# Kernel optimization log

Measured on AMD Instinct MI355X. Metric: run time of the kernel, lower is better.

Reference implementation:

```python
import jax, jax.numpy as jnp
import numpy as np

NUM_HEADS = 32
HEAD_DIM = 128
NUM_KV_HEADS = 8
SCALING = HEAD_DIM ** -0.5


def setup_inputs() -> dict:
    key = jax.random.key(0)
    kq, kk, kv = jax.random.split(key, 3)
    B, S = 2, 2048
    return {
        "query": jax.random.normal(kq, (B, S, NUM_HEADS * HEAD_DIM), dtype=jnp.float32),
        "key": jax.random.normal(kk, (B, S, NUM_KV_HEADS * HEAD_DIM), dtype=jnp.float32),
        "value": jax.random.normal(kv, (B, S, NUM_KV_HEADS * HEAD_DIM), dtype=jnp.float32),
    }


def reference(query, key, value):
    B, S, _ = query.shape
    n_rep = NUM_HEADS // NUM_KV_HEADS
    # [B, H, S, D]
    q = query.reshape(B, S, NUM_HEADS, HEAD_DIM).transpose(0, 2, 1, 3)
    k = key.reshape(B, S, NUM_KV_HEADS, HEAD_DIM).transpose(0, 2, 1, 3)
    v = value.reshape(B, S, NUM_KV_HEADS, HEAD_DIM).transpose(0, 2, 1, 3)
    # repeat_kv: (B, Hkv, S, D) -> (B, Hkv*n_rep, S, D)
    k = jnp.repeat(k, n_rep, axis=1)
    v = jnp.repeat(v, n_rep, axis=1)
    # attention scores [B, H, S, S]
    scores = jnp.einsum("bhqd,bhkd->bhqk", q, k) * SCALING
    causal = jnp.tril(jnp.ones((S, S), dtype=bool))
    scores = jnp.where(causal, scores, -jnp.inf)
    # softmax in fp32, cast back to query dtype
    attn = jax.nn.softmax(scores.astype(jnp.float32), axis=-1).astype(q.dtype)
    out = jnp.einsum("bhqk,bhkd->bhqd", attn, v)
    # back to [B, S, H*D]
    return out.transpose(0, 2, 1, 3).reshape(B, S, NUM_HEADS * HEAD_DIM)
```

## Files before the change

kernel.cpp:

```cpp
#include <hip/hip_runtime.h>

#define B_    2
#define S_    2048
#define H_    32
#define KVH_  8
#define D_    128
#define QB    128
#define KB    64
#define NT_   (S_ / KB)
#define SCALE2 0.12751743f
#define THR2  8.0f

typedef short  short8 __attribute__((ext_vector_type(8)));
typedef float  f32x4  __attribute__((ext_vector_type(4)));

__device__ inline unsigned short f2bf(float f) {
    unsigned int u = __float_as_uint(f);
    u += 0x7fffu + ((u >> 16) & 1u);
    return (unsigned short)(u >> 16);
}
__device__ __forceinline__ float exp2_fast(float x) {
    float r; asm("v_exp_f32 %0, %1" : "=v"(r) : "v"(x)); return r;
}
__device__ __forceinline__ unsigned int cvt_pk_bf16(float lo, float hi) {
    unsigned int r;
    asm("v_cvt_pk_bf16_f32 %0, %1, %2" : "=v"(r) : "v"(lo), "v"(hi));
    return r;
}

__global__ void prep_kernel(const float* __restrict__ k, const float* __restrict__ v,
                            unsigned short* __restrict__ kfb,
                            unsigned short* __restrict__ vfb) {
    __shared__ unsigned short Kt[64][136];
    __shared__ unsigned short Vt[64][132];
    const int t = threadIdx.x;
    const int kt = blockIdx.x, bkvh = blockIdx.y;
    const int b = bkvh >> 3, kvh = bkvh & 7;
    const size_t rs = KVH_ * D_;
    const float* ks = k + ((size_t)(b * S_ + kt * 64)) * rs + kvh * D_;
    const float* vs = v + ((size_t)(b * S_ + kt * 64)) * rs + kvh * D_;
    #pragma unroll
    for (int i = 0; i < 8; ++i) {
        const int row = (t >> 5) + i * 8;
        const int col = (t & 31) * 4;
        const float4 a = *(const float4*)(ks + (size_t)row * rs + col);
        const float4 c = *(const float4*)(vs + (size_t)row * rs + col);
        ushort4 wa, wc;
        wa.x = f2bf(a.x); wa.y = f2bf(a.y); wa.z = f2bf(a.z); wa.w = f2bf(a.w);
        wc.x = f2bf(c.x); wc.y = f2bf(c.y); wc.z = f2bf(c.z); wc.w = f2bf(c.w);
        *(ushort4*)&Kt[row][col] = wa;
        *(ushort4*)&Vt[row][col] = wc;
    }
    __syncthreads();
    const int lane = t & 63, m16 = lane & 15, quad = lane >> 4;
    unsigned short* kout = kfb + (size_t)(bkvh * NT_ + kt) * 16 * 512;
    unsigned short* vout = vfb + (size_t)(bkvh * NT_ + kt) * 16 * 512;
    #pragma unroll
    for (int i = 0; i < 4; ++i) {
        const int g = (t >> 6) * 4 + i;
        const int c = g >> 2, nt = g & 3;
        const short8 kk = *(const short8*)&Kt[nt * 16 + m16][c * 32 + quad * 8];
        *(short8*)(kout + g * 512 + lane * 8) = kk;
        const int c2 = g >> 3, dn = g & 7;
        short8 vv;
        #pragma unroll
        for (int j = 0; j < 8; ++j)
            vv[j] = (short)Vt[c2 * 32 + quad * 8 + j][dn * 16 + m16];
        *(short8*)(vout + g * 512 + lane * 8) = vv;
    }
}

#define KV_TILE_B 16384
#define BUF_B     32768
#define PSH_OFF   65536
#define SMEM_B    (PSH_OFF + 128 * 64 * 2)

__device__ __forceinline__ void gld16(const void* g, void* l) {
    __builtin_amdgcn_global_load_lds(
        (const __attribute__((address_space(1))) unsigned int*)g,
        (__attribute__((address_space(3))) unsigned int*)l, 16, 0, 0);
}

__global__ __launch_bounds__(512, 4) void fa9_kernel(
    const float* __restrict__ q, const unsigned short* __restrict__ kfb,
    const unsigned short* __restrict__ vfb, float* __restrict__ out) {

    __shared__ __align__(16) char smem[SMEM_B];
    unsigned short* Psh = (unsigned short*)(smem + PSH_OFF);

    const int t    = threadIdx.x;
    const int wave = t >> 6;
    const int lane = t & 63;
    const int m16  = lane & 15;
    const int quad = lane >> 4;

    const int bh  = blockIdx.y;
    const int b   = bh >> 5;
    const int h   = bh & 31;
    const int kvh = h >> 2;

    const char* kB = (const char*)kfb + (size_t)(b * KVH_ + kvh) * NT_ * KV_TILE_B;
    const char* vB = (const char*)vfb + (size_t)(b * KVH_ + kvh) * NT_ * KV_TILE_B;

    const int prow_base = (wave * 16 + m16) * 64;
    unsigned short* pw[4];
    #pragma unroll
    for (int nt = 0; nt < 4; ++nt)
        pw[nt] = Psh + prow_base + (((nt * 2 + (quad >> 1)) ^ (m16 & 7)) << 3) + (quad & 1) * 4;
    const unsigned short* pr0 = Psh + prow_base + (((quad)     ^ (m16 & 7)) << 3);
    const unsigned short* pr1 = Psh + prow_base + (((4 + quad) ^ (m16 & 7)) << 3);

    for (int half = 0; half < 2; ++half) {
        const int qtile = half ? (int)blockIdx.x : (S_ / QB - 1 - (int)blockIdx.x);
        const int qbase = qtile * QB;
        const int ktmax = 2 * qtile + 1;
        const int qrow  = qbase + wave * 16 + m16;

        if (half) __syncthreads();

        #pragma unroll
        for (int r = 0; r < 2; ++r) {
            gld16(kB + r * 8192 + t * 16, smem + r * 8192 + t * 16);
            gld16(vB + r * 8192 + t * 16, smem + KV_TILE_B + r * 8192 + t * 16);
        }

        short8 qf[4];
        {
            const float* qp = q + (size_t)(b * S_ + qrow) * (H_ * D_) + h * D_;
            #pragma unroll
            for (int c = 0; c < 4; ++c) {
                const float4 x0 = *(const float4*)(qp + c * 32 + quad * 8);
                const float4 x1 = *(const float4*)(qp + c * 32 + quad * 8 + 4);
                short8 f;
                f[0] = (short)f2bf(x0.x * SCALE2); f[1] = (short)f2bf(x0.y * SCALE2);
                f[2] = (short)f2bf(x0.z * SCALE2); f[3] = (short)f2bf(x0.w * SCALE2);
                f[4] = (short)f2bf(x1.x * SCALE2); f[5] = (short)f2bf(x1.y * SCALE2);
                f[6] = (short)f2bf(x1.z * SCALE2); f[7] = (short)f2bf(x1.w * SCALE2);
                qf[c] = f;
            }
        }

        f32x4 o[8];
        #pragma unroll
        for (int i = 0; i < 8; ++i) o[i] = (f32x4){0.f, 0.f, 0.f, 0.f};
        float m_q = -INFINITY, l_q = 0.f;

        __syncthreads();

        for (int ktt = 0; ktt <= ktmax; ++ktt) {
            const int kb  = ktt * KB;
            const int cur = ktt & 1;

            if (ktt < ktmax) {
                char* dst = smem + (cur ^ 1) * BUF_B + t * 16;
                const char* ks = kB + (size_t)(ktt + 1) * KV_TILE_B + t * 16;
                const char* vs = vB + (size_t)(ktt + 1) * KV_TILE_B + t * 16;
                #pragma unroll
                for (int r = 0; r < 2; ++r) {
                    gld16(ks + r * 8192, dst + r * 8192);
                    gld16(vs + r * 8192, dst + KV_TILE_B + r * 8192);
                }
            }
            const unsigned short* Kl = (const unsigned short*)(smem + cur * BUF_B);
            const unsigned short* Vl = Kl + KV_TILE_B / 2;

            f32x4 sa[4];
            #pragma unroll
            for (int nt = 0; nt < 4; ++nt) sa[nt] = (f32x4){0.f, 0.f, 0.f, 0.f};
            #pragma unroll
            for (int c = 0; c < 4; ++c) {
                short8 kf[4];
                #pragma unroll
                for (int nt = 0; nt < 4; ++nt)
                    kf[nt] = *(const short8*)(Kl + (c * 4 + nt) * 512 + lane * 8);
                #pragma unroll
                for (int nt = 0; nt < 4; ++nt)
                    sa[nt] = __builtin_amdgcn_mfma_f32_16x16x32_bf16(kf[nt], qf[c], sa[nt], 0, 0, 0);
            }

            const bool dodiag = (ktt >= 2 * qtile);
            float p[4][4];
            #pragma unroll
            for (int nt = 0; nt < 4; ++nt) {
                #pragma unroll
                for (int r = 0; r < 4; ++r) {
                    float sv = sa[nt][r];
                    if (dodiag) {
                        const int keyg = kb + nt * 16 + quad * 4 + r;
                        if (keyg > qrow) sv = -INFINITY;
                    }
                    p[nt][r] = sv;
                }
            }
            float mv;
            {
                float t0 = fmaxf(fmaxf(p[0][0], p[0][1]), fmaxf(p[0][2], p[0][3]));
                float t1 = fmaxf(fmaxf(p[1][0], p[1][1]), fmaxf(p[1][2], p[1][3]));
                float t2 = fmaxf(fmaxf(p[2][0], p[2][1]), fmaxf(p[2][2], p[2][3]));
                float t3 = fmaxf(fmaxf(p[3][0], p[3][1]), fmaxf(p[3][2], p[3][3]));
                mv = fmaxf(fmaxf(t0, t1), fmaxf(t2, t3));
                mv = fmaxf(mv, __shfl_xor(mv, 16));
                mv = fmaxf(mv, __shfl_xor(mv, 32));
            }
            if (__any(mv - m_q > THR2)) {
                const float mnew = fmaxf(m_q, mv);
                const float al = exp2_fast(m_q - mnew);
                m_q = mnew;
                l_q *= al;
                float alo[4];
                #pragma unroll
                for (int r = 0; r < 4; ++r)
                    alo[r] = __shfl(al, quad * 20 + r);
                #pragma unroll
                for (int dn = 0; dn < 8; ++dn)
                    #pragma unroll
                    for (int r = 0; r < 4; ++r) o[dn][r] *= alo[r];
            }
            #pragma unroll
            for (int nt = 0; nt < 4; ++nt) {
                const float e0 = exp2_fast(p[nt][0] - m_q);
                const float e1 = exp2_fast(p[nt][1] - m_q);
                const float e2 = exp2_fast(p[nt][2] - m_q);
                const float e3 = exp2_fast(p[nt][3] - m_q);
                l_q += (e0 + e1) + (e2 + e3);
                uint2 w;
                w.x = cvt_pk_bf16(e0, e1);
                w.y = cvt_pk_bf16(e2, e3);
                *(uint2*)pw[nt] = w;
            }
            asm volatile("s_waitcnt lgkmcnt(0)" ::: "memory");
            short8 pf[2];
            pf[0] = *(const short8*)pr0;
            pf[1] = *(const short8*)pr1;

            #pragma unroll
            for (int dn = 0; dn < 8; ++dn) {
                const short8 vv = *(const short8*)(Vl + dn * 512 + lane * 8);
                o[dn] = __builtin_amdgcn_mfma_f32_16x16x32_bf16(pf[0], vv, o[dn], 0, 0, 0);
            }
            #pragma unroll
            for (int dn = 0; dn < 8; ++dn) {
                const short8 vv = *(const short8*)(Vl + (8 + dn) * 512 + lane * 8);
                o[dn] = __builtin_amdgcn_mfma_f32_16x16x32_bf16(pf[1], vv, o[dn], 0, 0, 0);
            }

            __syncthreads();
        }

        float ls = l_q;
        ls += __shfl_xor(ls, 16);
        ls += __shfl_xor(ls, 32);
        const float inv_q = 1.f / ls;
        float inv[4];
        #pragma unroll
        for (int r = 0; r < 4; ++r)
            inv[r] = __shfl(inv_q, quad * 20 + r);

        float* Ot = (float*)smem + wave * (16 * 128);
        #pragma unroll
        for (int dn = 0; dn < 8; ++dn)
            #pragma unroll
            for (int r = 0; r < 4; ++r)
                Ot[(quad * 4 + r) * 128 + dn * 16 + m16] = o[dn][r] * inv[r];
        asm volatile("s_waitcnt lgkmcnt(0)" ::: "memory");
        float* og = out + (size_t)(b * S_ + qbase + wave * 16) * (H_ * D_) + h * D_;
        #pragma unroll
        for (int i = 0; i < 8; ++i) {
            const int row = (lane >> 5) + i * 2;
            const int col = (lane & 31) * 4;
            *(float4*)(og + (size_t)row * (H_ * D_) + col) = *(const float4*)(Ot + row * 128 + col);
        }
    }
}

extern "C" void kernel_launch(void* const* d_in, const int* in_sizes, int n_in,
                              void* d_out, int out_size, void* d_ws, size_t ws_size,
                              hipStream_t stream) {
    const float* q = (const float*)d_in[0];
    const float* k = (const float*)d_in[1];
    const float* v = (const float*)d_in[2];
    float* out = (float*)d_out;

    unsigned short* kfb = (unsigned short*)d_ws;
    unsigned short* vfb = (unsigned short*)d_ws + (size_t)B_ * KVH_ * S_ * D_;

    prep_kernel<<<dim3(NT_, B_ * KVH_), dim3(256), 0, stream>>>(k, v, kfb, vfb);
    fa9_kernel<<<dim3(S_ / QB / 2, B_ * H_), dim3(512), 0, stream>>>(q, kfb, vfb, out);
}
```

Baseline: 225.9 us.

## Restructure attention to 4-wave blocks with two query row-blocks per wave and 32-key tiles

The attention kernel drops from 8 waves to 4 waves per block. Each wave now handles two 16-row query blocks that share each K/V fragment load, and keys are streamed in 32-key sub-tiles with a smaller double buffer. The prep kernel is split so each block handles 32 keys, and the output layout is reordered to match. The paired-qtile load balancing is removed: each block processes one q tile, heaviest first. s_setprio is added around the MFMA sections. The aim is more fragment reuse per LDS read and less LDS per block. The costs are more register pressure, more loop iterations and barriers, and causal imbalance between blocks.

```diff
diff --git a/kernel.cpp b/kernel.cpp
--- a/kernel.cpp
+++ b/kernel.cpp
@@ -6,8 +6,7 @@
 #define KVH_  8
 #define D_    128
 #define QB    128
-#define KB    64
-#define NT_   (S_ / KB)
+#define NT_   (S_ / 64)
 #define SCALE2 0.12751743f
 #define THR2  8.0f
 
@@ -31,16 +30,17 @@
 __global__ void prep_kernel(const float* __restrict__ k, const float* __restrict__ v,
                             unsigned short* __restrict__ kfb,
                             unsigned short* __restrict__ vfb) {
-    __shared__ unsigned short Kt[64][136];
-    __shared__ unsigned short Vt[64][132];
+    __shared__ unsigned short Kt[32][136];
+    __shared__ unsigned short Vt[32][132];
     const int t = threadIdx.x;
-    const int kt = blockIdx.x, bkvh = blockIdx.y;
+    const int kt64 = blockIdx.x >> 1, sub = blockIdx.x & 1;
+    const int bkvh = blockIdx.y;
     const int b = bkvh >> 3, kvh = bkvh & 7;
     const size_t rs = KVH_ * D_;
-    const float* ks = k + ((size_t)(b * S_ + kt * 64)) * rs + kvh * D_;
-    const float* vs = v + ((size_t)(b * S_ + kt * 64)) * rs + kvh * D_;
-    #pragma unroll
-    for (int i = 0; i < 8; ++i) {
+    const float* ks = k + ((size_t)(b * S_ + kt64 * 64 + sub * 32)) * rs + kvh * D_;
+    const float* vs = v + ((size_t)(b * S_ + kt64 * 64 + sub * 32)) * rs + kvh * D_;
+    #pragma unroll
+    for (int i = 0; i < 4; ++i) {
         const int row = (t >> 5) + i * 8;
         const int col = (t & 31) * 4;
         const float4 a = *(const float4*)(ks + (size_t)row * rs + col);
@@ -53,27 +53,29 @@
     }
     __syncthreads();
     const int lane = t & 63, m16 = lane & 15, quad = lane >> 4;
-    unsigned short* kout = kfb + (size_t)(bkvh * NT_ + kt) * 16 * 512;
-    unsigned short* vout = vfb + (size_t)(bkvh * NT_ + kt) * 16 * 512;
-    #pragma unroll
-    for (int i = 0; i < 4; ++i) {
-        const int g = (t >> 6) * 4 + i;
-        const int c = g >> 2, nt = g & 3;
-        const short8 kk = *(const short8*)&Kt[nt * 16 + m16][c * 32 + quad * 8];
-        *(short8*)(kout + g * 512 + lane * 8) = kk;
-        const int c2 = g >> 3, dn = g & 7;
+    const int w = t >> 6;
+    unsigned short* kout = kfb + (size_t)(bkvh * NT_ + kt64) * 16 * 512;
+    unsigned short* vout = vfb + (size_t)(bkvh * NT_ + kt64) * 16 * 512;
+    #pragma unroll
+    for (int ntl = 0; ntl < 2; ++ntl) {
+        const short8 kk = *(const short8*)&Kt[ntl * 16 + m16][w * 32 + quad * 8];
+        *(short8*)(kout + (w * 4 + sub * 2 + ntl) * 512 + lane * 8) = kk;
+    }
+    #pragma unroll
+    for (int i = 0; i < 2; ++i) {
+        const int dn = w * 2 + i;
         short8 vv;
         #pragma unroll
         for (int j = 0; j < 8; ++j)
-            vv[j] = (short)Vt[c2 * 32 + quad * 8 + j][dn * 16 + m16];
-        *(short8*)(vout + g * 512 + lane * 8) = vv;
-    }
-}
-
-#define KV_TILE_B 16384
-#define BUF_B     32768
-#define PSH_OFF   65536
-#define SMEM_B    (PSH_OFF + 128 * 64 * 2)
+            vv[j] = (short)Vt[quad * 8 + j][dn * 16 + m16];
+        *(short8*)(vout + (sub * 8 + dn) * 512 + lane * 8) = vv;
+    }
+}
+
+#define TILE64_B 16384
+#define BUF_B    16384
+#define PSH_OFF  32768
+#define SMEM_B   (PSH_OFF + 128 * 64 * 2)
 
 __device__ __forceinline__ void gld16(const void* g, void* l) {
     __builtin_amdgcn_global_load_lds(
@@ -81,7 +83,7 @@
         (__attribute__((address_space(3))) unsigned int*)l, 16, 0, 0);
 }
 
-__global__ __launch_bounds__(512, 4) void fa9_kernel(
+__global__ __launch_bounds__(256, 3) void fa10_kernel(
     const float* __restrict__ q, const unsigned short* __restrict__ kfb,
     const unsigned short* __restrict__ vfb, float* __restrict__ out) {
 
@@ -94,119 +96,125 @@
     const int m16  = lane & 15;
     const int quad = lane >> 4;
 
+    const int qtile = 15 - (int)blockIdx.x;
+    const int qbase = qtile * QB;
+    const int ktmax = 4 * qtile + 3;
+
     const int bh  = blockIdx.y;
     const int b   = bh >> 5;
     const int h   = bh & 31;
     const int kvh = h >> 2;
 
-    const char* kB = (const char*)kfb + (size_t)(b * KVH_ + kvh) * NT_ * KV_TILE_B;
-    const char* vB = (const char*)vfb + (size_t)(b * KVH_ + kvh) * NT_ * KV_TILE_B;
-
-    const int prow_base = (wave * 16 + m16) * 64;
-    unsigned short* pw[4];
-    #pragma unroll
-    for (int nt = 0; nt < 4; ++nt)
-        pw[nt] = Psh + prow_base + (((nt * 2 + (quad >> 1)) ^ (m16 & 7)) << 3) + (quad & 1) * 4;
-    const unsigned short* pr0 = Psh + prow_base + (((quad)     ^ (m16 & 7)) << 3);
-    const unsigned short* pr1 = Psh + prow_base + (((4 + quad) ^ (m16 & 7)) << 3);
-
-    for (int half = 0; half < 2; ++half) {
-        const int qtile = half ? (int)blockIdx.x : (S_ / QB - 1 - (int)blockIdx.x);
-        const int qbase = qtile * QB;
-        const int ktmax = 2 * qtile + 1;
-        const int qrow  = qbase + wave * 16 + m16;
-
-        if (half) __syncthreads();
-
-        #pragma unroll
-        for (int r = 0; r < 2; ++r) {
-            gld16(kB + r * 8192 + t * 16, smem + r * 8192 + t * 16);
-            gld16(vB + r * 8192 + t * 16, smem + KV_TILE_B + r * 8192 + t * 16);
-        }
-
-        short8 qf[4];
-        {
-            const float* qp = q + (size_t)(b * S_ + qrow) * (H_ * D_) + h * D_;
+    const char* kB = (const char*)kfb + (size_t)(b * KVH_ + kvh) * NT_ * TILE64_B;
+    const char* vB = (const char*)vfb + (size_t)(b * KVH_ + kvh) * NT_ * TILE64_B;
+
+    const int inner = lane * 16;
+    const int g0 = wave;
+    const int kst0 = ((g0 >> 1) * 4 + (g0 & 1)) * 1024 + inner;
+    const int kst1 = (((g0 + 4) >> 1) * 4 + ((g0 + 4) & 1)) * 1024 + inner;
+
+    const int psh_row0 = (wave * 16 + m16) * 64;
+    unsigned short* pw0 = Psh + psh_row0 + ((((quad >> 1))     ^ (m16 & 7)) << 3) + (quad & 1) * 4;
+    unsigned short* pw1 = Psh + psh_row0 + (((2 + (quad >> 1)) ^ (m16 & 7)) << 3) + (quad & 1) * 4;
+    const unsigned short* pr = Psh + psh_row0 + ((quad ^ (m16 & 7)) << 3);
+
+    gld16(kB + kst0,          smem + t * 16);
+    gld16(kB + kst1,          smem + 4096 + t * 16);
+    gld16(vB + t * 16,        smem + 8192 + t * 16);
+    gld16(vB + 4096 + t * 16, smem + 12288 + t * 16);
+
+    const int qr0 = qbase + wave * 16 + m16;
+    const int qr1 = qr0 + 64;
+    short8 qf[2][4];
+    #pragma unroll
+    for (int rb = 0; rb < 2; ++rb) {
+        const float* qp = q + (size_t)(b * S_ + (rb ? qr1 : qr0)) * (H_ * D_) + h * D_;
+        #pragma unroll
+        for (int c = 0; c < 4; ++c) {
+            const float4 x0 = *(const float4*)(qp + c * 32 + quad * 8);
+            const float4 x1 = *(const float4*)(qp + c * 32 + quad * 8 + 4);
+            short8 f;
+            f[0] = (short)f2bf(x0.x * SCALE2); f[1] = (short)f2bf(x0.y * SCALE2);
+            f[2] = (short)f2bf(x0.z * SCALE2); f[3] = (short)f2bf(x0.w * SCALE2);
+            f[4] = (short)f2bf(x1.x * SCALE2); f[5] = (short)f2bf(x1.y * SCALE2);
+            f[6] = (short)f2bf(x1.z * SCALE2); f[7] = (short)f2bf(x1.w * SCALE2);
+            qf[rb][c] = f;
+        }
+    }
+
+    f32x4 o[2][8];
+    #pragma unroll
+    for (int rb = 0; rb < 2; ++rb)
+        #pragma unroll
+        for (int i = 0; i < 8; ++i) o[rb][i] = (f32x4){0.f, 0.f, 0.f, 0.f};
+    float m_q[2] = {-INFINITY, -INFINITY}, l_q[2] = {0.f, 0.f};
+
+    __syncthreads();
+
+    for (int ktt = 0; ktt <= ktmax; ++ktt) {
+        const int kb  = ktt * 32;
+        const int cur = ktt & 1;
+
+        if (ktt < ktmax) {
+            const int n = ktt + 1;
+            const char* kt_ = kB + (size_t)(n >> 1) * TILE64_B + (n & 1) * 2048;
+            const char* vt_ = vB + (size_t)(n >> 1) * TILE64_B + (n & 1) * 8192;
+            char* dst = smem + (n & 1) * BUF_B;
+            gld16(kt_ + kst0,          dst + t * 16);
+            gld16(kt_ + kst1,          dst + 4096 + t * 16);
+            gld16(vt_ + t * 16,        dst + 8192 + t * 16);
+            gld16(vt_ + 4096 + t * 16, dst + 12288 + t * 16);
+        }
+        const unsigned short* Kl = (const unsigned short*)(smem + cur * BUF_B);
+        const unsigned short* Vl = Kl + 4096;
+
+        f32x4 sa[2][2];
+        #pragma unroll
+        for (int rb = 0; rb < 2; ++rb)
             #pragma unroll
-            for (int c = 0; c < 4; ++c) {
-                const float4 x0 = *(const float4*)(qp + c * 32 + quad * 8);
-                const float4 x1 = *(const float4*)(qp + c * 32 + quad * 8 + 4);
-                short8 f;
-                f[0] = (short)f2bf(x0.x * SCALE2); f[1] = (short)f2bf(x0.y * SCALE2);
-                f[2] = (short)f2bf(x0.z * SCALE2); f[3] = (short)f2bf(x0.w * SCALE2);
-                f[4] = (short)f2bf(x1.x * SCALE2); f[5] = (short)f2bf(x1.y * SCALE2);
-                f[6] = (short)f2bf(x1.z * SCALE2); f[7] = (short)f2bf(x1.w * SCALE2);
-                qf[c] = f;
-            }
-        }
-
-        f32x4 o[8];
-        #pragma unroll
-        for (int i = 0; i < 8; ++i) o[i] = (f32x4){0.f, 0.f, 0.f, 0.f};
-        float m_q = -INFINITY, l_q = 0.f;
-
-        __syncthreads();
-
-        for (int ktt = 0; ktt <= ktmax; ++ktt) {
-            const int kb  = ktt * KB;
-            const int cur = ktt & 1;
-
-            if (ktt < ktmax) {
-                char* dst = smem + (cur ^ 1) * BUF_B + t * 16;
-                const char* ks = kB + (size_t)(ktt + 1) * KV_TILE_B + t * 16;
-                const char* vs = vB + (size_t)(ktt + 1) * KV_TILE_B + t * 16;
-                #pragma unroll
-                for (int r = 0; r < 2; ++r) {
-                    gld16(ks + r * 8192, dst + r * 8192);
-                    gld16(vs + r * 8192, dst + KV_TILE_B + r * 8192);
-                }
-            }
-            const unsigned short* Kl = (const unsigned short*)(smem + cur * BUF_B);
-            const unsigned short* Vl = Kl + KV_TILE_B / 2;
-
-            f32x4 sa[4];
+            for (int ntl = 0; ntl < 2; ++ntl) sa[rb][ntl] = (f32x4){0.f, 0.f, 0.f, 0.f};
+        __builtin_amdgcn_s_setprio(1);
+        #pragma unroll
+        for (int c = 0; c < 4; ++c) {
+            const short8 kf0 = *(const short8*)(Kl + (c * 2)     * 512 + lane * 8);
+            const short8 kf1 = *(const short8*)(Kl + (c * 2 + 1) * 512 + lane * 8);
+            sa[0][0] = __builtin_amdgcn_mfma_f32_16x16x32_bf16(kf0, qf[0][c], sa[0][0], 0, 0, 0);
+            sa[0][1] = __builtin_amdgcn_mfma_f32_16x16x32_bf16(kf1, qf[0][c], sa[0][1], 0, 0, 0);
+            sa[1][0] = __builtin_amdgcn_mfma_f32_16x16x32_bf16(kf0, qf[1][c], sa[1][0], 0, 0, 0);
+            sa[1][1] = __builtin_amdgcn_mfma_f32_16x16x32_bf16(kf1, qf[1][c], sa[1][1], 0, 0, 0);
+        }
+        __builtin_amdgcn_s_setprio(0);
+
+        #pragma unroll
+        for (int rb = 0; rb < 2; ++rb) {
+            const bool dodiag = (ktt >= 4 * qtile + 2 * rb);
+            const int  qr = rb ? qr1 : qr0;
+            float p[2][4];
             #pragma unroll
-            for (int nt = 0; nt < 4; ++nt) sa[nt] = (f32x4){0.f, 0.f, 0.f, 0.f};
-            #pragma unroll
-            for (int c = 0; c < 4; ++c) {
-                short8 kf[4];
-                #pragma unroll
-                for (int nt = 0; nt < 4; ++nt)
-                    kf[nt] = *(const short8*)(Kl + (c * 4 + nt) * 512 + lane * 8);
-                #pragma unroll
-                for (int nt = 0; nt < 4; ++nt)
-                    sa[nt] = __builtin_amdgcn_mfma_f32_16x16x32_bf16(kf[nt], qf[c], sa[nt], 0, 0, 0);
-            }
-
-            const bool dodiag = (ktt >= 2 * qtile);
-            float p[4][4];
-            #pragma unroll
-            for (int nt = 0; nt < 4; ++nt) {
+            for (int ntl = 0; ntl < 2; ++ntl) {
                 #pragma unroll
                 for (int r = 0; r < 4; ++r) {
-                    float sv = sa[nt][r];
+                    float sv = sa[rb][ntl][r];
                     if (dodiag) {
-                        const int keyg = kb + nt * 16 + quad * 4 + r;
-                        if (keyg > qrow) sv = -INFINITY;
+                        const int keyg = kb + ntl * 16 + quad * 4 + r;
+                        if (keyg > qr) sv = -INFINITY;
                     }
-                    p[nt][r] = sv;
+                    p[ntl][r] = sv;
                 }
             }
             float mv;
             {
-                float t0 = fmaxf(fmaxf(p[0][0], p[0][1]), fmaxf(p[0][2], p[0][3]));
-                float t1 = fmaxf(fmaxf(p[1][0], p[1][1]), fmaxf(p[1][2], p[1][3]));
-                float t2 = fmaxf(fmaxf(p[2][0], p[2][1]), fmaxf(p[2][2], p[2][3]));
-                float t3 = fmaxf(fmaxf(p[3][0], p[3][1]), fmaxf(p[3][2], p[3][3]));
-                mv = fmaxf(fmaxf(t0, t1), fmaxf(t2, t3));
+                const float t0 = fmaxf(fmaxf(p[0][0], p[0][1]), fmaxf(p[0][2], p[0][3]));
+                const float t1 = fmaxf(fmaxf(p[1][0], p[1][1]), fmaxf(p[1][2], p[1][3]));
+                mv = fmaxf(t0, t1);
                 mv = fmaxf(mv, __shfl_xor(mv, 16));
                 mv = fmaxf(mv, __shfl_xor(mv, 32));
             }
-            if (__any(mv - m_q > THR2)) {
-                const float mnew = fmaxf(m_q, mv);
-                const float al = exp2_fast(m_q - mnew);
-                m_q = mnew;
-                l_q *= al;
+            if (__any(mv - m_q[rb] > THR2)) {
+                const float mnew = fmaxf(m_q[rb], mv);
+                const float al = exp2_fast(m_q[rb] - mnew);
+                m_q[rb] = mnew;
+                l_q[rb] *= al;
                 float alo[4];
                 #pragma unroll
                 for (int r = 0; r < 4; ++r)
@@ -214,40 +222,47 @@
                 #pragma unroll
                 for (int dn = 0; dn < 8; ++dn)
                     #pragma unroll
-                    for (int r = 0; r < 4; ++r) o[dn][r] *= alo[r];
+                    for (int r = 0; r < 4; ++r) o[rb][dn][r] *= alo[r];
             }
-            #pragma unroll
-            for (int nt = 0; nt < 4; ++nt) {
-                const float e0 = exp2_fast(p[nt][0] - m_q);
-                const float e1 = exp2_fast(p[nt][1] - m_q);
-                const float e2 = exp2_fast(p[nt][2] - m_q);
-                const float e3 = exp2_fast(p[nt][3] - m_q);
-                l_q += (e0 + e1) + (e2 + e3);
-                uint2 w;
-                w.x = cvt_pk_bf16(e0, e1);
-                w.y = cvt_pk_bf16(e2, e3);
-                *(uint2*)pw[nt] = w;
+            {
+                const float e0 = exp2_fast(p[0][0] - m_q[rb]);
+                const float e1 = exp2_fast(p[0][1] - m_q[rb]);
+                const float e2 = exp2_fast(p[0][2] - m_q[rb]);
+                const float e3 = exp2_fast(p[0][3] - m_q[rb]);
+                const float f0 = exp2_fast(p[1][0] - m_q[rb]);
+                const float f1 = exp2_fast(p[1][1] - m_q[rb]);
+                const float f2 = exp2_fast(p[1][2] - m_q[rb]);
+                const float f3 = exp2_fast(p[1][3] - m_q[rb]);
+                l_q[rb] += ((e0 + e1) + (e2 + e3)) + ((f0 + f1) + (f2 + f3));
+                uint2 w0, w1;
+                w0.x = cvt_pk_bf16(e0, e1); w0.y = cvt_pk_bf16(e2, e3);
+                w1.x = cvt_pk_bf16(f0, f1); w1.y = cvt_pk_bf16(f2, f3);
+                *(uint2*)(pw0 + rb * 4096) = w0;
+                *(uint2*)(pw1 + rb * 4096) = w1;
             }
-            asm volatile("s_waitcnt lgkmcnt(0)" ::: "memory");
-            short8 pf[2];
-            pf[0] = *(const short8*)pr0;
-            pf[1] = *(const short8*)pr1;
-
-            #pragma unroll
-            for (int dn = 0; dn < 8; ++dn) {
-                const short8 vv = *(const short8*)(Vl + dn * 512 + lane * 8);
-                o[dn] = __builtin_amdgcn_mfma_f32_16x16x32_bf16(pf[0], vv, o[dn], 0, 0, 0);
-            }
-            #pragma unroll
-            for (int dn = 0; dn < 8; ++dn) {
-                const short8 vv = *(const short8*)(Vl + (8 + dn) * 512 + lane * 8);
-                o[dn] = __builtin_amdgcn_mfma_f32_16x16x32_bf16(pf[1], vv, o[dn], 0, 0, 0);
-            }
-
-            __syncthreads();
-        }
-
-        float ls = l_q;
+        }
+
+        asm volatile("s_waitcnt lgkmcnt(0)" ::: "memory");
+        short8 pf[2];
+        pf[0] = *(const short8*)pr;
+        pf[1] = *(const short8*)(pr + 4096);
+
+        __builtin_amdgcn_s_setprio(1);
+        #pragma unroll
+        for (int dn = 0; dn < 8; ++dn) {
+            const short8 vv = *(const short8*)(Vl + dn * 512 + lane * 8);
+            o[0][dn] = __builtin_amdgcn_mfma_f32_16x16x32_bf16(pf[0], vv, o[0][dn], 0, 0, 0);
+            o[1][dn] = __builtin_amdgcn_mfma_f32_16x16x32_bf16(pf[1], vv, o[1][dn], 0, 0, 0);
+        }
+        __builtin_amdgcn_s_setprio(0);
+
+        __syncthreads();
+    }
+
+    float* Ot = (float*)smem + wave * 2048;
+    #pragma unroll
+    for (int rb = 0; rb < 2; ++rb) {
+        float ls = l_q[rb];
         ls += __shfl_xor(ls, 16);
         ls += __shfl_xor(ls, 32);
         const float inv_q = 1.f / ls;
@@ -255,15 +270,13 @@
         #pragma unroll
         for (int r = 0; r < 4; ++r)
             inv[r] = __shfl(inv_q, quad * 20 + r);
-
-        float* Ot = (float*)smem + wave * (16 * 128);
         #pragma unroll
         for (int dn = 0; dn < 8; ++dn)
             #pragma unroll
             for (int r = 0; r < 4; ++r)
-                Ot[(quad * 4 + r) * 128 + dn * 16 + m16] = o[dn][r] * inv[r];
+                Ot[(quad * 4 + r) * 128 + dn * 16 + m16] = o[rb][dn][r] * inv[r];
         asm volatile("s_waitcnt lgkmcnt(0)" ::: "memory");
-        float* og = out + (size_t)(b * S_ + qbase + wave * 16) * (H_ * D_) + h * D_;
+        float* og = out + (size_t)(b * S_ + qbase + rb * 64 + wave * 16) * (H_ * D_) + h * D_;
         #pragma unroll
         for (int i = 0; i < 8; ++i) {
             const int row = (lane >> 5) + i * 2;
@@ -284,6 +297,6 @@
     unsigned short* kfb = (unsigned short*)d_ws;
     unsigned short* vfb = (unsigned short*)d_ws + (size_t)B_ * KVH_ * S_ * D_;
 
-    prep_kernel<<<dim3(NT_, B_ * KVH_), dim3(256), 0, stream>>>(k, v, kfb, vfb);
-    fa9_kernel<<<dim3(S_ / QB / 2, B_ * H_), dim3(512), 0, stream>>>(q, kfb, vfb, out);
-}
+    prep_kernel<<<dim3(NT_ * 2, B_ * KVH_), dim3(256), 0, stream>>>(k, v, kfb, vfb);
+    fa10_kernel<<<dim3(16, B_ * H_), dim3(256), 0, stream>>>(q, kfb, vfb, out);
+}
```

Result: slower. 302.6 us (+33.9%).

## Halve waves per block, each wave computes two 16-row query sub-blocks

Applied to the files above, without the earlier changes.

The block drops from 8 waves to 4 and each wave now handles two 16-row query blocks (rows r and r+64). Every K and V fragment read from LDS therefore feeds two MFMAs, halving LDS traffic per FLOP, and the causal mask is applied per sub-block. MFMA sections are wrapped in s_setprio to favour matrix issue. The cost is roughly double the accumulator and score registers per wave and fewer waves to hide latency. Launch bounds change to (256,2) to match.

```diff
diff --git a/kernel.cpp b/kernel.cpp
--- a/kernel.cpp
+++ b/kernel.cpp
@@ -6,8 +6,7 @@
 #define KVH_  8
 #define D_    128
 #define QB    128
-#define KB    64
-#define NT_   (S_ / KB)
+#define NT_   (S_ / 64)
 #define SCALE2 0.12751743f
 #define THR2  8.0f
 
@@ -70,10 +69,10 @@
     }
 }
 
-#define KV_TILE_B 16384
-#define BUF_B     32768
-#define PSH_OFF   65536
-#define SMEM_B    (PSH_OFF + 128 * 64 * 2)
+#define TILE_B  16384
+#define BUF_B   32768
+#define PSH_OFF 65536
+#define SMEM_B  (PSH_OFF + 128 * 64 * 2)
 
 __device__ __forceinline__ void gld16(const void* g, void* l) {
     __builtin_amdgcn_global_load_lds(
@@ -81,7 +80,7 @@
         (__attribute__((address_space(3))) unsigned int*)l, 16, 0, 0);
 }
 
-__global__ __launch_bounds__(512, 4) void fa9_kernel(
+__global__ __launch_bounds__(256, 2) void fa11_kernel(
     const float* __restrict__ q, const unsigned short* __restrict__ kfb,
     const unsigned short* __restrict__ vfb, float* __restrict__ out) {
 
@@ -99,34 +98,36 @@
     const int h   = bh & 31;
     const int kvh = h >> 2;
 
-    const char* kB = (const char*)kfb + (size_t)(b * KVH_ + kvh) * NT_ * KV_TILE_B;
-    const char* vB = (const char*)vfb + (size_t)(b * KVH_ + kvh) * NT_ * KV_TILE_B;
-
-    const int prow_base = (wave * 16 + m16) * 64;
+    const char* kB = (const char*)kfb + (size_t)(b * KVH_ + kvh) * NT_ * TILE_B;
+    const char* vB = (const char*)vfb + (size_t)(b * KVH_ + kvh) * NT_ * TILE_B;
+
+    const int psh_row = (wave * 16 + m16) * 64;
     unsigned short* pw[4];
     #pragma unroll
     for (int nt = 0; nt < 4; ++nt)
-        pw[nt] = Psh + prow_base + (((nt * 2 + (quad >> 1)) ^ (m16 & 7)) << 3) + (quad & 1) * 4;
-    const unsigned short* pr0 = Psh + prow_base + (((quad)     ^ (m16 & 7)) << 3);
-    const unsigned short* pr1 = Psh + prow_base + (((4 + quad) ^ (m16 & 7)) << 3);
+        pw[nt] = Psh + psh_row + (((nt * 2 + (quad >> 1)) ^ (m16 & 7)) << 3) + (quad & 1) * 4;
+    const unsigned short* pr0 = Psh + psh_row + (((quad)     ^ (m16 & 7)) << 3);
+    const unsigned short* pr1 = Psh + psh_row + (((4 + quad) ^ (m16 & 7)) << 3);
 
     for (int half = 0; half < 2; ++half) {
-        const int qtile = half ? (int)blockIdx.x : (S_ / QB - 1 - (int)blockIdx.x);
+        const int qtile = half ? (int)blockIdx.x : (15 - (int)blockIdx.x);
         const int qbase = qtile * QB;
         const int ktmax = 2 * qtile + 1;
-        const int qrow  = qbase + wave * 16 + m16;
 
         if (half) __syncthreads();
 
         #pragma unroll
-        for (int r = 0; r < 2; ++r) {
-            gld16(kB + r * 8192 + t * 16, smem + r * 8192 + t * 16);
-            gld16(vB + r * 8192 + t * 16, smem + KV_TILE_B + r * 8192 + t * 16);
+        for (int r = 0; r < 4; ++r) {
+            gld16(kB + r * 4096 + t * 16, smem + r * 4096 + t * 16);
+            gld16(vB + r * 4096 + t * 16, smem + 16384 + r * 4096 + t * 16);
         }
 
-        short8 qf[4];
-        {
-            const float* qp = q + (size_t)(b * S_ + qrow) * (H_ * D_) + h * D_;
+        const int qr0 = qbase + wave * 16 + m16;
+        const int qr1 = qr0 + 64;
+        short8 qf[2][4];
+        #pragma unroll
+        for (int rb = 0; rb < 2; ++rb) {
+            const float* qp = q + (size_t)(b * S_ + (rb ? qr1 : qr0)) * (H_ * D_) + h * D_;
             #pragma unroll
             for (int c = 0; c < 4; ++c) {
                 const float4 x0 = *(const float4*)(qp + c * 32 + quad * 8);
@@ -136,37 +137,42 @@
                 f[2] = (short)f2bf(x0.z * SCALE2); f[3] = (short)f2bf(x0.w * SCALE2);
                 f[4] = (short)f2bf(x1.x * SCALE2); f[5] = (short)f2bf(x1.y * SCALE2);
                 f[6] = (short)f2bf(x1.z * SCALE2); f[7] = (short)f2bf(x1.w * SCALE2);
-                qf[c] = f;
+                qf[rb][c] = f;
             }
         }
 
-        f32x4 o[8];
-        #pragma unroll
-        for (int i = 0; i < 8; ++i) o[i] = (f32x4){0.f, 0.f, 0.f, 0.f};
-        float m_q = -INFINITY, l_q = 0.f;
+        f32x4 o[2][8];
+        #pragma unroll
+        for (int rb = 0; rb < 2; ++rb)
+            #pragma unroll
+            for (int i = 0; i < 8; ++i) o[rb][i] = (f32x4){0.f, 0.f, 0.f, 0.f};
+        float m_q[2] = {-INFINITY, -INFINITY}, l_q[2] = {0.f, 0.f};
 
         __syncthreads();
 
         for (int ktt = 0; ktt <= ktmax; ++ktt) {
-            const int kb  = ktt * KB;
+            const int kb  = ktt * 64;
             const int cur = ktt & 1;
 
             if (ktt < ktmax) {
+                const char* ks = kB + (size_t)(ktt + 1) * TILE_B + t * 16;
+                const char* vs = vB + (size_t)(ktt + 1) * TILE_B + t * 16;
                 char* dst = smem + (cur ^ 1) * BUF_B + t * 16;
-                const char* ks = kB + (size_t)(ktt + 1) * KV_TILE_B + t * 16;
-                const char* vs = vB + (size_t)(ktt + 1) * KV_TILE_B + t * 16;
-                #pragma unroll
-                for (int r = 0; r < 2; ++r) {
-                    gld16(ks + r * 8192, dst + r * 8192);
-                    gld16(vs + r * 8192, dst + KV_TILE_B + r * 8192);
+                #pragma unroll
+                for (int r = 0; r < 4; ++r) {
+                    gld16(ks + r * 4096, dst + r * 4096);
+                    gld16(vs + r * 4096, dst + 16384 + r * 4096);
                 }
             }
             const unsigned short* Kl = (const unsigned short*)(smem + cur * BUF_B);
-            const unsigned short* Vl = Kl + KV_TILE_B / 2;
-
-            f32x4 sa[4];
-            #pragma unroll
-            for (int nt = 0; nt < 4; ++nt) sa[nt] = (f32x4){0.f, 0.f, 0.f, 0.f};
+            const unsigned short* Vl = Kl + 8192;
+
+            f32x4 sa[2][4];
+            #pragma unroll
+            for (int rb = 0; rb < 2; ++rb)
+                #pragma unroll
+                for (int nt = 0; nt < 4; ++nt) sa[rb][nt] = (f32x4){0.f, 0.f, 0.f, 0.f};
+            __builtin_amdgcn_s_setprio(1);
             #pragma unroll
             for (int c = 0; c < 4; ++c) {
                 short8 kf[4];
@@ -174,101 +180,114 @@
                 for (int nt = 0; nt < 4; ++nt)
                     kf[nt] = *(const short8*)(Kl + (c * 4 + nt) * 512 + lane * 8);
                 #pragma unroll
-                for (int nt = 0; nt < 4; ++nt)
-                    sa[nt] = __builtin_amdgcn_mfma_f32_16x16x32_bf16(kf[nt], qf[c], sa[nt], 0, 0, 0);
-            }
-
-            const bool dodiag = (ktt >= 2 * qtile);
-            float p[4][4];
-            #pragma unroll
-            for (int nt = 0; nt < 4; ++nt) {
-                #pragma unroll
-                for (int r = 0; r < 4; ++r) {
-                    float sv = sa[nt][r];
-                    if (dodiag) {
-                        const int keyg = kb + nt * 16 + quad * 4 + r;
-                        if (keyg > qrow) sv = -INFINITY;
+                for (int nt = 0; nt < 4; ++nt) {
+                    sa[0][nt] = __builtin_amdgcn_mfma_f32_16x16x32_bf16(kf[nt], qf[0][c], sa[0][nt], 0, 0, 0);
+                    sa[1][nt] = __builtin_amdgcn_mfma_f32_16x16x32_bf16(kf[nt], qf[1][c], sa[1][nt], 0, 0, 0);
+                }
+            }
+            __builtin_amdgcn_s_setprio(0);
+
+            #pragma unroll
+            for (int rb = 0; rb < 2; ++rb) {
+                const bool dodiag = (ktt >= 2 * qtile + rb);
+                const int  qr = rb ? qr1 : qr0;
+                float p[4][4];
+                #pragma unroll
+                for (int nt = 0; nt < 4; ++nt) {
+                    #pragma unroll
+                    for (int r = 0; r < 4; ++r) {
+                        float sv = sa[rb][nt][r];
+                        if (dodiag) {
+                            const int keyg = kb + nt * 16 + quad * 4 + r;
+                            if (keyg > qr) sv = -INFINITY;
+                        }
+                        p[nt][r] = sv;
                     }
-                    p[nt][r] = sv;
-                }
-            }
-            float mv;
-            {
-                float t0 = fmaxf(fmaxf(p[0][0], p[0][1]), fmaxf(p[0][2], p[0][3]));
-                float t1 = fmaxf(fmaxf(p[1][0], p[1][1]), fmaxf(p[1][2], p[1][3]));
-                float t2 = fmaxf(fmaxf(p[2][0], p[2][1]), fmaxf(p[2][2], p[2][3]));
-                float t3 = fmaxf(fmaxf(p[3][0], p[3][1]), fmaxf(p[3][2], p[3][3]));
-                mv = fmaxf(fmaxf(t0, t1), fmaxf(t2, t3));
-                mv = fmaxf(mv, __shfl_xor(mv, 16));
-                mv = fmaxf(mv, __shfl_xor(mv, 32));
-            }
-            if (__any(mv - m_q > THR2)) {
-                const float mnew = fmaxf(m_q, mv);
-                const float al = exp2_fast(m_q - mnew);
-                m_q = mnew;
-                l_q *= al;
-                float alo[4];
-                #pragma unroll
-                for (int r = 0; r < 4; ++r)
-                    alo[r] = __shfl(al, quad * 20 + r);
-                #pragma unroll
-                for (int dn = 0; dn < 8; ++dn)
+                }
+                float mv;
+                {
+                    const float t0 = fmaxf(fmaxf(p[0][0], p[0][1]), fmaxf(p[0][2], p[0][3]));
+                    const float t1 = fmaxf(fmaxf(p[1][0], p[1][1]), fmaxf(p[1][2], p[1][3]));
+                    const float t2 = fmaxf(fmaxf(p[2][0], p[2][1]), fmaxf(p[2][2], p[2][3]));
+                    const float t3 = fmaxf(fmaxf(p[3][0], p[3][1]), fmaxf(p[3][2], p[3][3]));
+                    mv = fmaxf(fmaxf(t0, t1), fmaxf(t2, t3));
+                    mv = fmaxf(mv, __shfl_xor(mv, 16));
+                    mv = fmaxf(mv, __shfl_xor(mv, 32));
+                }
+                if (__any(mv - m_q[rb] > THR2)) {
+                    const float mnew = fmaxf(m_q[rb], mv);
+                    const float al = exp2_fast(m_q[rb] - mnew);
+                    m_q[rb] = mnew;
+                    l_q[rb] *= al;
+                    float alo[4];
                     #pragma unroll
-                    for (int r = 0; r < 4; ++r) o[dn][r] *= alo[r];
-            }
-            #pragma unroll
-            for (int nt = 0; nt < 4; ++nt) {
-                const float e0 = exp2_fast(p[nt][0] - m_q);
-                const float e1 = exp2_fast(p[nt][1] - m_q);
-                const float e2 = exp2_fast(p[nt][2] - m_q);
-                const float e3 = exp2_fast(p[nt][3] - m_q);
-                l_q += (e0 + e1) + (e2 + e3);
-                uint2 w;
-                w.x = cvt_pk_bf16(e0, e1);
-                w.y = cvt_pk_bf16(e2, e3);
-                *(uint2*)pw[nt] = w;
-            }
+                    for (int r = 0; r < 4; ++r)
+                        alo[r] = __shfl(al, quad * 20 + r);
+                    #pragma unroll
+                    for (int dn = 0; dn < 8; ++dn)
+                        #pragma unroll
+                        for (int r = 0; r < 4; ++r) o[rb][dn][r] *= alo[r];
+                }
+                #pragma unroll
+                for (int nt = 0; nt < 4; ++nt) {
+                    const float e0 = exp2_fast(p[nt][0] - m_q[rb]);
+                    const float e1 = exp2_fast(p[nt][1] - m_q[rb]);
+                    const float e2 = exp2_fast(p[nt][2] - m_q[rb]);
+                    const float e3 = exp2_fast(p[nt][3] - m_q[rb]);
+                    l_q[rb] += (e0 + e1) + (e2 + e3);
+                    uint2 w;
+                    w.x = cvt_pk_bf16(e0, e1);
+                    w.y = cvt_pk_bf16(e2, e3);
+                    *(uint2*)(pw[nt] + rb * 4096) = w;
+                }
+            }
+
             asm volatile("s_waitcnt lgkmcnt(0)" ::: "memory");
-            short8 pf[2];
-            pf[0] = *(const short8*)pr0;
-            pf[1] = *(const short8*)pr1;
-
-            #pragma unroll
-            for (int dn = 0; dn < 8; ++dn) {
-                const short8 vv = *(const short8*)(Vl + dn * 512 + lane * 8);
-                o[dn] = __builtin_amdgcn_mfma_f32_16x16x32_bf16(pf[0], vv, o[dn], 0, 0, 0);
-            }
-            #pragma unroll
-            for (int dn = 0; dn < 8; ++dn) {
-                const short8 vv = *(const short8*)(Vl + (8 + dn) * 512 + lane * 8);
-                o[dn] = __builtin_amdgcn_mfma_f32_16x16x32_bf16(pf[1], vv, o[dn], 0, 0, 0);
-            }
+            short8 pf[2][2];
+            pf[0][0] = *(const short8*)pr0;
+            pf[0][1] = *(const short8*)pr1;
+            pf[1][0] = *(const short8*)(pr0 + 4096);
+            pf[1][1] = *(const short8*)(pr1 + 4096);
+
+            __builtin_amdgcn_s_setprio(1);
+            #pragma unroll
+            for (int c2 = 0; c2 < 2; ++c2) {
+                #pragma unroll
+                for (int dn = 0; dn < 8; ++dn) {
+                    const short8 vv = *(const short8*)(Vl + (c2 * 8 + dn) * 512 + lane * 8);
+                    o[0][dn] = __builtin_amdgcn_mfma_f32_16x16x32_bf16(pf[0][c2], vv, o[0][dn], 0, 0, 0);
+                    o[1][dn] = __builtin_amdgcn_mfma_f32_16x16x32_bf16(pf[1][c2], vv, o[1][dn], 0, 0, 0);
+                }
+            }
+            __builtin_amdgcn_s_setprio(0);
 
             __syncthreads();
         }
 
-        float ls = l_q;
-        ls += __shfl_xor(ls, 16);
-        ls += __shfl_xor(ls, 32);
-        const float inv_q = 1.f / ls;
-        float inv[4];
-        #pragma unroll
-        for (int r = 0; r < 4; ++r)
-            inv[r] = __shfl(inv_q, quad * 20 + r);
-
-        float* Ot = (float*)smem + wave * (16 * 128);
-        #pragma unroll
-        for (int dn = 0; dn < 8; ++dn)
+        float* Ot = (float*)smem + wave * 2048;
+        #pragma unroll
+        for (int rb = 0; rb < 2; ++rb) {
+            float ls = l_q[rb];
+            ls += __shfl_xor(ls, 16);
+            ls += __shfl_xor(ls, 32);
+            const float inv_q = 1.f / ls;
+            float inv[4];
             #pragma unroll
             for (int r = 0; r < 4; ++r)
-                Ot[(quad * 4 + r) * 128 + dn * 16 + m16] = o[dn][r] * inv[r];
-        asm volatile("s_waitcnt lgkmcnt(0)" ::: "memory");
-        float* og = out + (size_t)(b * S_ + qbase + wave * 16) * (H_ * D_) + h * D_;
-        #pragma unroll
-        for (int i = 0; i < 8; ++i) {
-            const int row = (lane >> 5) + i * 2;
-            const int col = (lane & 31) * 4;
-            *(float4*)(og + (size_t)row * (H_ * D_) + col) = *(const float4*)(Ot + row * 128 + col);
+                inv[r] = __shfl(inv_q, quad * 20 + r);
+            #pragma unroll
+            for (int dn = 0; dn < 8; ++dn)
+                #pragma unroll
+                for (int r = 0; r < 4; ++r)
+                    Ot[(quad * 4 + r) * 128 + dn * 16 + m16] = o[rb][dn][r] * inv[r];
+            asm volatile("s_waitcnt lgkmcnt(0)" ::: "memory");
+            float* og = out + (size_t)(b * S_ + qbase + rb * 64 + wave * 16) * (H_ * D_) + h * D_;
+            #pragma unroll
+            for (int i = 0; i < 8; ++i) {
+                const int row = (lane >> 5) + i * 2;
+                const int col = (lane & 31) * 4;
+                *(float4*)(og + (size_t)row * (H_ * D_) + col) = *(const float4*)(Ot + row * 128 + col);
+            }
         }
     }
 }
@@ -285,5 +304,5 @@
     unsigned short* vfb = (unsigned short*)d_ws + (size_t)B_ * KVH_ * S_ * D_;
 
     prep_kernel<<<dim3(NT_, B_ * KVH_), dim3(256), 0, stream>>>(k, v, kfb, vfb);
-    fa9_kernel<<<dim3(S_ / QB / 2, B_ * H_), dim3(512), 0, stream>>>(q, kfb, vfb, out);
-}
+    fa11_kernel<<<dim3(8, B_ * H_), dim3(256), 0, stream>>>(q, kfb, vfb, out);
+}
```

After: 226.4 us. About the same (+0.2%).
